# Kernel optimization log

Measured on AMD Instinct MI355X. Metric: run time of the kernel, lower is better.

The kernel has to match this reference:

```python
import jax, jax.numpy as jnp
import numpy as np

ALPHA = 1.0      # init: alpha
N_LAMBDA = 1.0   # init: n_lambda
EPS = 1e-6


def _sq_cdist(a, b):
    # a: [B,N,3], b: [B,M,3] -> [B,N,M] squared euclidean distances
    return (jnp.sum(a * a, -1)[:, :, None]
            + jnp.sum(b * b, -1)[:, None, :]
            - 2.0 * jnp.einsum('bnd,bmd->bnm', a, b))


def setup_inputs() -> dict:
    key = jax.random.key(0)
    k1, k2 = jax.random.split(key)
    B, N = 4, 8192
    gts = jax.random.normal(k1, (B, N, 3), dtype=jnp.float32)
    preds = jax.random.normal(k2, (B, N, 3), dtype=jnp.float32)
    return {"gts": gts, "preds": preds}


def reference(gts, preds):
    x, gt = preds.astype(jnp.float32), gts.astype(jnp.float32)
    B, n_x, _ = x.shape
    n_gt = gt.shape[1]
    frac_12 = n_x / n_gt
    frac_21 = n_gt / n_x

    d = _sq_cdist(gt, x)              # [B, n_gt, n_x]
    idx1 = jnp.argmin(d, axis=2)      # [B, n_gt], NN of each gt point in x
    idx2 = jnp.argmin(d, axis=1)      # [B, n_x],  NN of each x point in gt
    brow = jnp.arange(B)[:, None]

    # NN squared distances recomputed via gather (same values as the min)
    dist1 = jnp.sum((gt - x[brow, idx1]) ** 2, -1)   # [B, n_gt]
    dist2 = jnp.sum((x - gt[brow, idx2]) ** 2, -1)   # [B, n_x]

    exp_dist1 = jnp.exp(-dist1 * ALPHA)
    exp_dist2 = jnp.exp(-dist2 * ALPHA)

    # density counts: how many gt points chose each x point (and vice versa)
    count1 = jnp.zeros((B, n_x), jnp.float32).at[brow, idx1].add(1.0)
    weight1 = count1[brow, idx1] ** N_LAMBDA
    weight1 = frac_21 / (weight1 + EPS)
    loss1 = jnp.mean(1.0 - exp_dist1 * weight1, axis=1)

    count2 = jnp.zeros((B, n_gt), jnp.float32).at[brow, idx2].add(1.0)
    weight2 = count2[brow, idx2] ** N_LAMBDA
    weight2 = frac_12 / (weight2 + EPS)
    loss2 = jnp.mean(1.0 - exp_dist2 * weight2, axis=1)

    return (loss1 + loss2) / 2.0
```

## Files before the change

kernel.cpp:

```cpp
#include <hip/hip_runtime.h>
#include <math.h>


#define NPTS   8192
#define BLK    256
#define QPB    512
#define TPS    1024
#define TILES  (TPS / 32)
#define NSLICE (NPTS / TPS)
#define QCH    (NPTS / QPB)
#define GRP    256
#define NGRP   (NPTS / GRP)
#define FQ     64

typedef __attribute__((ext_vector_type(8)))  short short8;
typedef __attribute__((ext_vector_type(16))) float float16v;

__device__ inline void bsplit(float x, unsigned short& h, unsigned short& l) {
    const unsigned int u = __float_as_uint(x);
    const unsigned short hh = (unsigned short)(u >> 16);
    const float lf = x - __uint_as_float((unsigned int)hh << 16);
    h = hh;
    l = (unsigned short)(__float_as_uint(lf) >> 16);
}

__device__ inline short8 make_bfrag(float qx, float qy, float qz, int khalf) {
    const float q2 = fmaf(qx, qx, fmaf(qy, qy, qz * qz));
    unsigned short shx, slx, shy, sly, shz, slz, h2q, l2q;
    bsplit(-2.0f * qx, shx, slx); bsplit(-2.0f * qy, shy, sly);
    bsplit(-2.0f * qz, shz, slz); bsplit(q2, h2q, l2q);
    union { short8 v; unsigned short s[8]; } bu;
    if (khalf == 0) {
        bu.s[0]=shx; bu.s[1]=shy; bu.s[2]=shz; bu.s[3]=slx; bu.s[4]=sly; bu.s[5]=slz; bu.s[6]=shx; bu.s[7]=shy;
    } else {
        bu.s[0]=shz; bu.s[1]=0x3F80; bu.s[2]=0x3F80; bu.s[3]=h2q; bu.s[4]=l2q; bu.s[5]=0; bu.s[6]=0; bu.s[7]=0;
    }
    return bu.v;
}

__device__ inline float tree16(const float16v& a) {
    const float t0 = fminf(fminf(a[0],  a[1]),  a[2]);
    const float t1 = fminf(fminf(a[3],  a[4]),  a[5]);
    const float t2 = fminf(fminf(a[6],  a[7]),  a[8]);
    const float t3 = fminf(fminf(a[9],  a[10]), a[11]);
    const float t4 = fminf(fminf(a[12], a[13]), a[14]);
    return fminf(fminf(fminf(t0, t1), a[15]), fminf(fminf(t2, t3), t4));
}

__global__ __launch_bounds__(BLK, 4) void dacl_partial(
    const float* __restrict__ gts, const float* __restrict__ preds,
    float* __restrict__ slot, int* __restrict__ cnt, int B, int N)
{
    const int bz  = blockIdx.z;
    const int dir = bz / B;
    const int b   = bz - dir * B;
    const int total = 2 * B * N;

    if (blockIdx.y == 0) {
        const int per = total / (QCH * 2 * B);
        int* p = cnt + (blockIdx.x + QCH * bz) * per;
        for (int k = threadIdx.x; k < per; k += BLK) p[k] = 0;
    }

    const float* __restrict__ q = (dir == 0 ? gts : preds) + (size_t)b * N * 3;
    const float* __restrict__ t = (dir == 0 ? preds : gts) + (size_t)b * N * 3;

    __shared__ short8 frag[TILES * 64];

    const int sbase = blockIdx.y * TPS;
    for (int rep = 0; rep < TPS / BLK; ++rep) {
        const int tgt = rep * BLK + threadIdx.x;
        const int j   = sbase + tgt;
        const float tx = t[3 * j], ty = t[3 * j + 1], tz = t[3 * j + 2];
        const float t2 = fmaf(tx, tx, fmaf(ty, ty, tz * tz));
        unsigned short hx, lx, hy, ly, hz, lz, h2, l2;
        bsplit(tx, hx, lx); bsplit(ty, hy, ly); bsplit(tz, hz, lz); bsplit(t2, h2, l2);
        union { short8 v; unsigned short s[8]; } k0, k1;
        k0.s[0]=hx; k0.s[1]=hy; k0.s[2]=hz; k0.s[3]=hx; k0.s[4]=hy; k0.s[5]=hz; k0.s[6]=lx; k0.s[7]=ly;
        k1.s[0]=lz; k1.s[1]=h2; k1.s[2]=l2; k1.s[3]=0x3F80; k1.s[4]=0x3F80; k1.s[5]=0; k1.s[6]=0; k1.s[7]=0;
        const int tile = tgt >> 5, row = tgt & 31;
        frag[tile * 64 + row]      = k0.v;
        frag[tile * 64 + 32 + row] = k1.v;
    }

    const int lane = threadIdx.x & 63;
    const int wave = threadIdx.x >> 6;
    const int kh   = lane >> 5;
    const int qiA  = blockIdx.x * QPB + wave * 32 + (lane & 31);
    const int qiB  = qiA + 128;
    const int qiC  = qiA + 256;
    const int qiD  = qiA + 384;
    const short8 bfragA = make_bfrag(q[3*qiA], q[3*qiA+1], q[3*qiA+2], kh);
    const short8 bfragB = make_bfrag(q[3*qiB], q[3*qiB+1], q[3*qiB+2], kh);
    const short8 bfragC = make_bfrag(q[3*qiC], q[3*qiC+1], q[3*qiC+2], kh);
    const short8 bfragD = make_bfrag(q[3*qiD], q[3*qiD+1], q[3*qiD+2], kh);

    __syncthreads();

    const float16v zz = {0.f,0.f,0.f,0.f, 0.f,0.f,0.f,0.f,
                         0.f,0.f,0.f,0.f, 0.f,0.f,0.f,0.f};
    const size_t gqA = (size_t)bz * N + qiA;
    float gminA = 3.402823466e38f, gminB = 3.402823466e38f;
    float gminC = 3.402823466e38f, gminD = 3.402823466e38f;

    #pragma unroll 2
    for (int tile = 0; tile < TILES; ++tile) {
        const short8 av = frag[tile * 64 + lane];
        const float16v aA = __builtin_amdgcn_mfma_f32_32x32x16_bf16(av, bfragA, zz, 0, 0, 0);
        const float16v aB = __builtin_amdgcn_mfma_f32_32x32x16_bf16(av, bfragB, zz, 0, 0, 0);
        const float16v aC = __builtin_amdgcn_mfma_f32_32x32x16_bf16(av, bfragC, zz, 0, 0, 0);
        const float16v aD = __builtin_amdgcn_mfma_f32_32x32x16_bf16(av, bfragD, zz, 0, 0, 0);
        gminA = fminf(gminA, tree16(aA));
        gminB = fminf(gminB, tree16(aB));
        gminC = fminf(gminC, tree16(aC));
        gminD = fminf(gminD, tree16(aD));
        if ((tile & 7) == 7) {
            const size_t rbase =
                (size_t)(blockIdx.y * (TILES / 8) + (tile >> 3)) * total;
            const float oA = fminf(gminA, __shfl_xor(gminA, 32, 64));
            const float oB = fminf(gminB, __shfl_xor(gminB, 32, 64));
            const float oC = fminf(gminC, __shfl_xor(gminC, 32, 64));
            const float oD = fminf(gminD, __shfl_xor(gminD, 32, 64));
            if (lane < 32) {
                slot[rbase + gqA]       = oA;
                slot[rbase + gqA + 128] = oB;
                slot[rbase + gqA + 256] = oC;
                slot[rbase + gqA + 384] = oD;
            }
            gminA = 3.402823466e38f; gminB = 3.402823466e38f;
            gminC = 3.402823466e38f; gminD = 3.402823466e38f;
        }
    }
}

__device__ inline float sq3(float x, float y, float z) {
    return fmaf(x, x, fmaf(y, y, z * z));
}

#define DIST8(V0,V1,V2,V3,V4,V5,BASE)                                          \
    do {                                                                       \
        const float d0 = sq3(qx-(V0).x, qy-(V0).y, qz-(V0).z);                 \
        const float d1 = sq3(qx-(V0).w, qy-(V1).x, qz-(V1).y);                 \
        const float d2 = sq3(qx-(V1).z, qy-(V1).w, qz-(V2).x);                 \
        const float d3 = sq3(qx-(V2).y, qy-(V2).z, qz-(V2).w);                 \
        const float d4 = sq3(qx-(V3).x, qy-(V3).y, qz-(V3).z);                 \
        const float d5 = sq3(qx-(V3).w, qy-(V4).x, qz-(V4).y);                 \
        const float d6 = sq3(qx-(V4).z, qy-(V4).w, qz-(V5).x);                 \
        const float d7 = sq3(qx-(V5).y, qy-(V5).z, qz-(V5).w);                 \
        best = min(best, (__float_as_uint(d0) & 0xFFFFFF00u) | (unsigned)((BASE)+0)); \
        best = min(best, (__float_as_uint(d1) & 0xFFFFFF00u) | (unsigned)((BASE)+1)); \
        best = min(best, (__float_as_uint(d2) & 0xFFFFFF00u) | (unsigned)((BASE)+2)); \
        best = min(best, (__float_as_uint(d3) & 0xFFFFFF00u) | (unsigned)((BASE)+3)); \
        best = min(best, (__float_as_uint(d4) & 0xFFFFFF00u) | (unsigned)((BASE)+4)); \
        best = min(best, (__float_as_uint(d5) & 0xFFFFFF00u) | (unsigned)((BASE)+5)); \
        best = min(best, (__float_as_uint(d6) & 0xFFFFFF00u) | (unsigned)((BASE)+6)); \
        best = min(best, (__float_as_uint(d7) & 0xFFFFFF00u) | (unsigned)((BASE)+7)); \
    } while (0)

__global__ __launch_bounds__(BLK) void dacl_merge(
    const float* __restrict__ gts, const float* __restrict__ preds,
    float* __restrict__ slot, int* __restrict__ cnt,
    float* __restrict__ out, int out_size, int B, int N)
{
    const int tid  = threadIdx.x;
    const int lane = tid & 63;
    const int wv   = tid >> 6;
    const int total = 2 * B * N;
    const int g0   = blockIdx.x * FQ;
    const int bz   = g0 / N;
    const int dir  = bz / B;
    const int b    = bz - dir * B;
    const float* __restrict__ q = (dir == 0 ? gts : preds) + (size_t)b * N * 3;
    const float* __restrict__ t = (dir == 0 ? preds : gts) + (size_t)b * N * 3;

    __shared__ unsigned int smin[FQ];
    __shared__ unsigned int skey[FQ];

    if (blockIdx.x == 0 && tid < out_size) out[tid] = 0.0f;
    if (tid < FQ) { smin[tid] = 0xFFFFFFFFu; skey[tid] = 0xFFFFFFFFu; }
    __syncthreads();

    const int g = g0 + lane;

    {
        unsigned int pk = 0xFFFFFFFFu;
        #pragma unroll
        for (int s = wv * 8; s < wv * 8 + 8; ++s) {
            const unsigned int ub0 = __float_as_uint(slot[(size_t)s * total + g]);
            const unsigned int ub  = ((int)ub0 < 0) ? ~ub0 : (ub0 | 0x80000000u);
            pk = min(pk, (ub & 0xFFFFFFE0u) | (unsigned int)s);
        }
        atomicMin(&smin[lane], pk);
    }
    __syncthreads();
    const int gr = (int)(smin[lane] & 31u);

    const float qx = q[3 * (g - bz * N)], qy = q[3 * (g - bz * N) + 1],
                qz = q[3 * (g - bz * N) + 2];
    {
        const float4* __restrict__ tb4 =
            (const float4*)(t + (size_t)gr * GRP * 3) + wv * 48;
        unsigned int best = 0xFFFFFFFFu;
        #pragma unroll
        for (int c = 0; c < 8; ++c) {
            const float4 v0 = tb4[c * 6 + 0];
            const float4 v1 = tb4[c * 6 + 1];
            const float4 v2 = tb4[c * 6 + 2];
            const float4 v3 = tb4[c * 6 + 3];
            const float4 v4 = tb4[c * 6 + 4];
            const float4 v5 = tb4[c * 6 + 5];
            DIST8(v0, v1, v2, v3, v4, v5, wv * 64 + c * 8);
        }
        atomicMin(&skey[lane], best);
    }
    __syncthreads();

    if (tid < FQ) {
        const unsigned int key = skey[tid];
        const int idxg = (int)(smin[tid] & 31u) * GRP + (int)(key & 255u);
        slot[g0 + tid]                 = __uint_as_float(key & 0xFFFFFF00u);
        ((int*)slot)[total + g0 + tid] = idxg;
        atomicAdd(&cnt[bz * N + idxg], 1);
    }
}

__global__ __launch_bounds__(256) void dacl_loss(
    const float* __restrict__ slot, const int* __restrict__ cnt,
    float* __restrict__ out, int B, int N)
{
    const int g  = blockIdx.x * 256 + threadIdx.x;
    const int total = 2 * B * N;
    const int bz = g / N;
    const int b  = bz - (bz / B) * B;

    const float d   = slot[g];
    const int   idx = ((const int*)slot)[total + g];
    const float c   = (float)cnt[bz * N + idx];
    float sv = 1.0f - expf(-d) / (c + 1e-6f);
    #pragma unroll
    for (int off = 32; off > 0; off >>= 1) sv += __shfl_down(sv, off, 64);
    if ((threadIdx.x & 63) == 0)
        atomicAdd(&out[b], sv / (2.0f * (float)N));
}

extern "C" void kernel_launch(void* const* d_in, const int* in_sizes, int n_in,
                              void* d_out, int out_size, void* d_ws, size_t ws_size,
                              hipStream_t stream)
{
    const float* gts   = (const float*)d_in[0];
    const float* preds = (const float*)d_in[1];

    const int N = NPTS;
    const int B = in_sizes[0] / (N * 3);

    const size_t nTot = (size_t)2 * B * N;
    float* slot = (float*)d_ws;
    int*   cnt  = (int*)((char*)d_ws + (size_t)NGRP * nTot * sizeof(float));

    dim3 gA(QCH, NSLICE, 2 * B);
    dacl_partial<<<gA, BLK, 0, stream>>>(gts, preds, slot, cnt, B, N);

    dacl_merge<<<(int)(nTot / FQ), BLK, 0, stream>>>(
        gts, preds, slot, cnt, (float*)d_out, out_size, B, N);

    dacl_loss<<<(int)(nTot / 256), 256, 0, stream>>>(
        slot, cnt, (float*)d_out, B, N);
}
```

Before: 113.4 us.

## Track winning 32-point tile in MFMA pass to narrow exact refinement

The MFMA coarse pass now records which of the 8 tiles in each 256-point group produced the minimum, packing the tile index into the low bits of an order-preserving key. The refinement kernel then recomputes exact distances for only the 32 candidates in that tile instead of the whole 256-point group. This cuts refinement loads and FMAs by 8x, but adds a compare/select per tile in the hot MFMA loop. Because the winner is picked from bf16-split approximate distances, a near-tie across tiles could now choose a different nearest neighbour than the exact one.

```diff
diff --git a/kernel.cpp b/kernel.cpp
--- a/kernel.cpp
+++ b/kernel.cpp
@@ -45,6 +45,12 @@
     const float t3 = fminf(fminf(a[9],  a[10]), a[11]);
     const float t4 = fminf(fminf(a[12], a[13]), a[14]);
     return fminf(fminf(fminf(t0, t1), a[15]), fminf(fminf(t2, t3), t4));
+}
+
+__device__ inline unsigned int packkey(float g, int tl) {
+    unsigned int u = __float_as_uint(g);
+    u = ((int)u < 0) ? ~u : (u | 0x80000000u);
+    return (u & 0xFFFFFF00u) | (unsigned int)tl;
 }
 
 __global__ __launch_bounds__(BLK, 4) void dacl_partial(
@@ -100,8 +106,10 @@
     const float16v zz = {0.f,0.f,0.f,0.f, 0.f,0.f,0.f,0.f,
                          0.f,0.f,0.f,0.f, 0.f,0.f,0.f,0.f};
     const size_t gqA = (size_t)bz * N + qiA;
+    unsigned int* __restrict__ slotU = (unsigned int*)slot;
     float gminA = 3.402823466e38f, gminB = 3.402823466e38f;
     float gminC = 3.402823466e38f, gminD = 3.402823466e38f;
+    int tlA = 0, tlB = 0, tlC = 0, tlD = 0;
 
     #pragma unroll 2
     for (int tile = 0; tile < TILES; ++tile) {
@@ -110,25 +118,34 @@
         const float16v aB = __builtin_amdgcn_mfma_f32_32x32x16_bf16(av, bfragB, zz, 0, 0, 0);
         const float16v aC = __builtin_amdgcn_mfma_f32_32x32x16_bf16(av, bfragC, zz, 0, 0, 0);
         const float16v aD = __builtin_amdgcn_mfma_f32_32x32x16_bf16(av, bfragD, zz, 0, 0, 0);
-        gminA = fminf(gminA, tree16(aA));
-        gminB = fminf(gminB, tree16(aB));
-        gminC = fminf(gminC, tree16(aC));
-        gminD = fminf(gminD, tree16(aD));
+        const float tA = tree16(aA);
+        const float tB = tree16(aB);
+        const float tC = tree16(aC);
+        const float tD = tree16(aD);
+        tlA = (tA < gminA) ? (tile & 7) : tlA;  gminA = fminf(gminA, tA);
+        tlB = (tB < gminB) ? (tile & 7) : tlB;  gminB = fminf(gminB, tB);
+        tlC = (tC < gminC) ? (tile & 7) : tlC;  gminC = fminf(gminC, tC);
+        tlD = (tD < gminD) ? (tile & 7) : tlD;  gminD = fminf(gminD, tD);
         if ((tile & 7) == 7) {
             const size_t rbase =
                 (size_t)(blockIdx.y * (TILES / 8) + (tile >> 3)) * total;
-            const float oA = fminf(gminA, __shfl_xor(gminA, 32, 64));
-            const float oB = fminf(gminB, __shfl_xor(gminB, 32, 64));
-            const float oC = fminf(gminC, __shfl_xor(gminC, 32, 64));
-            const float oD = fminf(gminD, __shfl_xor(gminD, 32, 64));
+            const unsigned int kA = packkey(gminA, tlA);
+            const unsigned int kB = packkey(gminB, tlB);
+            const unsigned int kC = packkey(gminC, tlC);
+            const unsigned int kD = packkey(gminD, tlD);
+            const unsigned int oA = min(kA, (unsigned int)__shfl_xor((int)kA, 32, 64));
+            const unsigned int oB = min(kB, (unsigned int)__shfl_xor((int)kB, 32, 64));
+            const unsigned int oC = min(kC, (unsigned int)__shfl_xor((int)kC, 32, 64));
+            const unsigned int oD = min(kD, (unsigned int)__shfl_xor((int)kD, 32, 64));
             if (lane < 32) {
-                slot[rbase + gqA]       = oA;
-                slot[rbase + gqA + 128] = oB;
-                slot[rbase + gqA + 256] = oC;
-                slot[rbase + gqA + 384] = oD;
+                slotU[rbase + gqA]       = oA;
+                slotU[rbase + gqA + 128] = oB;
+                slotU[rbase + gqA + 256] = oC;
+                slotU[rbase + gqA + 384] = oD;
             }
             gminA = 3.402823466e38f; gminB = 3.402823466e38f;
             gminC = 3.402823466e38f; gminD = 3.402823466e38f;
+            tlA = 0; tlB = 0; tlC = 0; tlD = 0;
         }
     }
 }
@@ -181,43 +198,42 @@
     __syncthreads();
 
     const int g = g0 + lane;
+    const unsigned int* __restrict__ slotU = (const unsigned int*)slot;
 
     {
         unsigned int pk = 0xFFFFFFFFu;
         #pragma unroll
-        for (int s = wv * 8; s < wv * 8 + 8; ++s) {
-            const unsigned int ub0 = __float_as_uint(slot[(size_t)s * total + g]);
-            const unsigned int ub  = ((int)ub0 < 0) ? ~ub0 : (ub0 | 0x80000000u);
-            pk = min(pk, (ub & 0xFFFFFFE0u) | (unsigned int)s);
-        }
+        for (int s = wv * 8; s < wv * 8 + 8; ++s)
+            pk = min(pk, slotU[(size_t)s * total + g] | ((unsigned int)s << 3));
         atomicMin(&smin[lane], pk);
     }
     __syncthreads();
-    const int gr = (int)(smin[lane] & 31u);
+    const unsigned int sel = smin[lane];
+    const int gr = (int)((sel >> 3) & 31u);
+    const int tl = (int)(sel & 7u);
 
     const float qx = q[3 * (g - bz * N)], qy = q[3 * (g - bz * N) + 1],
                 qz = q[3 * (g - bz * N) + 2];
     {
         const float4* __restrict__ tb4 =
-            (const float4*)(t + (size_t)gr * GRP * 3) + wv * 48;
+            (const float4*)(t + (size_t)(gr * GRP + tl * 32) * 3) + wv * 6;
         unsigned int best = 0xFFFFFFFFu;
-        #pragma unroll
-        for (int c = 0; c < 8; ++c) {
-            const float4 v0 = tb4[c * 6 + 0];
-            const float4 v1 = tb4[c * 6 + 1];
-            const float4 v2 = tb4[c * 6 + 2];
-            const float4 v3 = tb4[c * 6 + 3];
-            const float4 v4 = tb4[c * 6 + 4];
-            const float4 v5 = tb4[c * 6 + 5];
-            DIST8(v0, v1, v2, v3, v4, v5, wv * 64 + c * 8);
-        }
+        const float4 v0 = tb4[0];
+        const float4 v1 = tb4[1];
+        const float4 v2 = tb4[2];
+        const float4 v3 = tb4[3];
+        const float4 v4 = tb4[4];
+        const float4 v5 = tb4[5];
+        DIST8(v0, v1, v2, v3, v4, v5, wv * 8);
         atomicMin(&skey[lane], best);
     }
     __syncthreads();
 
     if (tid < FQ) {
         const unsigned int key = skey[tid];
-        const int idxg = (int)(smin[tid] & 31u) * GRP + (int)(key & 255u);
+        const unsigned int sl  = smin[tid];
+        const int idxg = (int)((sl >> 3) & 31u) * GRP + (int)(sl & 7u) * 32
+                       + (int)(key & 255u);
         slot[g0 + tid]                 = __uint_as_float(key & 0xFFFFFF00u);
         ((int*)slot)[total + g0 + tid] = idxg;
         atomicAdd(&cnt[bz * N + idxg], 1);
```

Result: faster. 101.5 us (-10.5%).
